# Optimization experiments

Hardware: AMD Instinct MI355X
Metric: run time of the kernel (lower is better)

Reference implementation:

```python
import jax, jax.numpy as jnp
import numpy as np

H = 64  # hidden size
IN = 1  # input size


def setup_inputs() -> dict:
    key = jax.random.key(0)
    ks = jax.random.split(key, 8)
    B, T = 4096, 512
    s_ih = 1.0 / np.sqrt(H)
    return {
        "x": jax.random.normal(ks[0], (B, T, IN), dtype=jnp.float32),
        # PyTorch LSTM params, gate order (i, f, g, o)
        "W_ih": jax.random.uniform(ks[1], (4 * H, IN), jnp.float32, -s_ih, s_ih),
        "W_hh": jax.random.uniform(ks[2], (4 * H, H), jnp.float32, -s_ih, s_ih),
        "b_ih": jax.random.uniform(ks[3], (4 * H,), jnp.float32, -s_ih, s_ih),
        "b_hh": jax.random.uniform(ks[4], (4 * H,), jnp.float32, -s_ih, s_ih),
        "W_fc": jax.random.uniform(ks[5], (1, H), jnp.float32, -s_ih, s_ih),
        "b_fc": jax.random.uniform(ks[6], (1,), jnp.float32, -s_ih, s_ih),
    }


def reference(x, W_ih, W_hh, b_ih, b_hh, W_fc, b_fc):
    B = x.shape[0]
    b = b_ih + b_hh  # fused bias, [4H]

    def step(carry, xt):
        h, c = carry  # [B,H], [B,H]
        gates = xt @ W_ih.T + h @ W_hh.T + b  # [B,4H]
        i, f, g, o = jnp.split(gates, 4, axis=-1)
        i = jax.nn.sigmoid(i)
        f = jax.nn.sigmoid(f)
        g = jnp.tanh(g)
        o = jax.nn.sigmoid(o)
        c = f * c + i * g
        h = o * jnp.tanh(c)
        return (h, c), None

    h0 = jnp.zeros((B, H), dtype=x.dtype)
    c0 = jnp.zeros((B, H), dtype=x.dtype)
    xs = jnp.swapaxes(x, 0, 1)  # [T,B,IN]
    (h_last, _), _ = jax.lax.scan(step, (h0, c0), xs)
    # fc applied to out[:, -1, :] == h_last
    return h_last @ W_fc.T + b_fc  # [B,1]
```

## Files before the change

### kernel.cpp

```cpp
#include <hip/hip_runtime.h>

#define T_STEPS 512
#define BT 16
#define XSTRIDE 524
#define HS2 136

typedef __attribute__((ext_vector_type(8))) short bf16x8;
typedef __attribute__((ext_vector_type(4))) float f32x4;
typedef __attribute__((ext_vector_type(4))) unsigned u32x4;

__device__ __forceinline__ short f2bf(float f) {
    union { float f; unsigned u; } v; v.f = f;
    unsigned r = v.u + 0x7fffu + ((v.u >> 16) & 1u);
    return (short)(r >> 16);
}
__device__ __forceinline__ float bf2f(short s) {
    union { float f; unsigned u; } v;
    v.u = ((unsigned)(unsigned short)s) << 16;
    return v.f;
}
__device__ __forceinline__ float ubits(unsigned u) {
    union { unsigned u; float f; } v; v.u = u; return v.f;
}
__device__ __forceinline__ float exp2_fast(float x) {
#if __has_builtin(__builtin_amdgcn_exp2f)
    return __builtin_amdgcn_exp2f(x);
#else
    return __expf(x * 0.69314718056f);
#endif
}

#define L2E 1.44269504089f
#define C2  2.88539008178f

__global__ __launch_bounds__(256, 1) void lstm_persist(
    const float* __restrict__ x,
    const float* __restrict__ W_ih,
    const float* __restrict__ W_hh,
    const float* __restrict__ b_ih,
    const float* __restrict__ b_hh,
    const float* __restrict__ W_fc,
    const float* __restrict__ b_fc,
    float* __restrict__ out)
{
    __shared__ __align__(16) float x_lds[BT * XSTRIDE];
    __shared__ __align__(16) short hbuf[2][BT][HS2];

    const int tid  = threadIdx.x;
    const int wave = tid >> 6;
    const int lane = tid & 63;
    const int l15  = lane & 15;
    const int quad = lane >> 4;
    const int b0   = blockIdx.x * BT;

    {
        const float* xg = x + (size_t)b0 * T_STEPS;
        #pragma unroll
        for (int i = 0; i < 8; ++i) {
            int f4 = tid + i * 256;
            int b  = f4 >> 7;
            int t4 = f4 & 127;
            float4 v = reinterpret_cast<const float4*>(xg + (size_t)b * T_STEPS)[t4];
            reinterpret_cast<float4*>(&x_lds[b * XSTRIDE + t4 * 4])[0] = v;
        }
    }
    {
        short* p = &hbuf[0][0][0];
        for (int i = tid; i < BT * HS2; i += 256) p[i] = 0;
        if (tid < BT) x_lds[tid * XSTRIDE + 512] = 0.f;
        if (tid >= 256 - 3 * BT && tid < 256) {
            int b = (tid - (256 - 3 * BT)) / 3, j = (tid - (256 - 3 * BT)) % 3;
            x_lds[b * XSTRIDE + 513 + j] = 0.f;
        }
    }

    const float scg[4] = { -L2E, -L2E, -C2, -L2E };
    bf16x8 Wv[4][4];
    f32x4 bias4[4], wih4[4];
    #pragma unroll
    for (int g = 0; g < 4; ++g) {
        int na = g * 64 + wave * 16 + l15;
        #pragma unroll
        for (int j = 0; j < 4; ++j) {
            int m = (wave + j) & 3;
            const float* wr = W_hh + na * 64 + m * 16 + quad * 4;
            bf16x8 a;
            #pragma unroll
            for (int jj = 0; jj < 4; ++jj) {
                short h16 = f2bf(wr[jj] * scg[g]);
                a[jj]     = h16;
                a[jj + 4] = h16;
            }
            Wv[g][j] = a;
        }
        #pragma unroll
        for (int r = 0; r < 4; ++r) {
            int n = g * 64 + wave * 16 + quad * 4 + r;
            bias4[g][r] = scg[g] * (b_ih[n] + b_hh[n]);
            wih4[g][r]  = scg[g] * W_ih[n];
        }
    }

    f32x4 ct4 = {0.f, 0.f, 0.f, 0.f};
    const int hoff = l15 * HS2 + quad * 8;
    const int off1 = hoff + 32 * ((wave + 1) & 3);
    const int off2 = hoff + 32 * ((wave + 2) & 3);
    const int off3 = hoff + 32 * ((wave + 3) & 3);
    const int w32  = l15 * (HS2 / 2) + (wave * 4 + quad) * 4;
    const f32x4* xrow4 = reinterpret_cast<const f32x4*>(&x_lds[l15 * XSTRIDE]);

    const f32x4 vone  = {1.f, 1.f, 1.f, 1.f};
    const f32x4 vnC2  = {-C2, -C2, -C2, -C2};
    const f32x4 vC2   = {C2, C2, C2, C2};
    const f32x4 v40   = {40.f, 40.f, 40.f, 40.f};

    u32x4 hw = {0u, 0u, 0u, 0u};

    __syncthreads();

    f32x4 xq = xrow4[0];
    f32x4 iv[4];
    {
        f32x4 xv4 = {xq[0], xq[0], xq[0], xq[0]};
        #pragma unroll
        for (int g = 0; g < 4; ++g)
            iv[g] = __builtin_elementwise_fma(wih4[g], xv4, bias4[g]);
    }

    for (int tg = 0; tg < T_STEPS / 4; ++tg) {
        f32x4 xqn = xrow4[tg + 1];
        #pragma unroll
        for (int u = 0; u < 4; ++u) {
            const int rb = u & 1, wb = rb ^ 1;
            const short* hb = &hbuf[rb][0][0];

            bf16x8 b1 = *reinterpret_cast<const bf16x8*>(hb + off1);
            bf16x8 b2 = *reinterpret_cast<const bf16x8*>(hb + off2);
            bf16x8 b3 = *reinterpret_cast<const bf16x8*>(hb + off3);
            bf16x8 bself;
            __builtin_memcpy(&bself, &hw, 16);

            f32x4 acc[4];
            #pragma unroll
            for (int g = 0; g < 4; ++g)
                acc[g] = __builtin_amdgcn_mfma_f32_16x16x32_bf16(Wv[g][0], bself, iv[g], 0, 0, 0);
            #pragma unroll
            for (int g = 0; g < 4; ++g)
                acc[g] = __builtin_amdgcn_mfma_f32_16x16x32_bf16(Wv[g][1], b1, acc[g], 0, 0, 0);
            #pragma unroll
            for (int g = 0; g < 4; ++g)
                acc[g] = __builtin_amdgcn_mfma_f32_16x16x32_bf16(Wv[g][2], b2, acc[g], 0, 0, 0);
            #pragma unroll
            for (int g = 0; g < 4; ++g)
                acc[g] = __builtin_amdgcn_mfma_f32_16x16x32_bf16(Wv[g][3], b3, acc[g], 0, 0, 0);

            {
                float xn = (u < 3) ? xq[u + 1] : xqn[0];
                f32x4 xn4 = {xn, xn, xn, xn};
                #pragma unroll
                for (int g = 0; g < 4; ++g)
                    iv[g] = __builtin_elementwise_fma(wih4[g], xn4, bias4[g]);
            }

            f32x4 ei, ef, eg, eo;
            #pragma unroll
            for (int r = 0; r < 4; ++r) {
                ei[r] = exp2_fast(acc[0][r]);
                ef[r] = exp2_fast(acc[1][r]);
                eg[r] = exp2_fast(acc[2][r]);
                eo[r] = exp2_fast(acc[3][r]);
            }
            f32x4 Ai = vone + ei, Af = vone + ef, Ag = vone + eg, Ao = vone + eo;
            f32x4 P   = Ai * Ag;
            f32x4 PAF = P * Af;
            f32x4 rP;
            #pragma unroll
            for (int r = 0; r < 4; ++r) rP[r] = __builtin_amdgcn_rcpf(PAF[r]);
            f32x4 tg4 = __builtin_elementwise_fma(vnC2, eg, vC2);
            f32x4 num = __builtin_elementwise_fma(ct4, P, tg4 * Af);
            f32x4 cn  = num * rP;
            ct4 = cn;
            f32x4 mm = __builtin_elementwise_min(-cn, v40);
            f32x4 ec;
            #pragma unroll
            for (int r = 0; r < 4; ++r) ec[r] = exp2_fast(mm[r]);
            f32x4 tc  = vone - ec;
            f32x4 den = Ao * (vone + ec);
            f32x4 rden;
            #pragma unroll
            for (int r = 0; r < 4; ++r) rden[r] = __builtin_amdgcn_rcpf(den[r]);
            f32x4 hv = tc * rden;

            unsigned hi01, hi23, lo01, lo23;
            asm("v_cvt_pk_bf16_f32 %0, %1, %2" : "=v"(hi01) : "v"(hv[0]), "v"(hv[1]));
            asm("v_cvt_pk_bf16_f32 %0, %1, %2" : "=v"(hi23) : "v"(hv[2]), "v"(hv[3]));
            f32x4 hif = { ubits(hi01 << 16), ubits(hi01 & 0xffff0000u),
                          ubits(hi23 << 16), ubits(hi23 & 0xffff0000u) };
            f32x4 l4 = hv - hif;
            asm("v_cvt_pk_bf16_f32 %0, %1, %2" : "=v"(lo01) : "v"(l4[0]), "v"(l4[1]));
            asm("v_cvt_pk_bf16_f32 %0, %1, %2" : "=v"(lo23) : "v"(l4[2]), "v"(l4[3]));
            hw = (u32x4){ hi01, hi23, lo01, lo23 };
            *reinterpret_cast<u32x4*>(reinterpret_cast<unsigned*>(&hbuf[wb][0][0]) + w32) = hw;

            __syncthreads();
        }
        xq = xqn;
    }

    if (tid < 16) {
        int b = tid;
        float s = b_fc[0];
        #pragma unroll 4
        for (int k = 0; k < 64; ++k) {
            int blk = k >> 2, j = k & 3;
            float hv = bf2f(hbuf[0][b][blk * 8 + j]) + bf2f(hbuf[0][b][blk * 8 + 4 + j]);
            s += hv * W_fc[k];
        }
        out[b0 + b] = s;
    }
}

extern "C" void kernel_launch(void* const* d_in, const int* in_sizes, int n_in,
                              void* d_out, int out_size, void* d_ws, size_t ws_size,
                              hipStream_t stream) {
    const float* x    = (const float*)d_in[0];
    const float* W_ih = (const float*)d_in[1];
    const float* W_hh = (const float*)d_in[2];
    const float* b_ih = (const float*)d_in[3];
    const float* b_hh = (const float*)d_in[4];
    const float* W_fc = (const float*)d_in[5];
    const float* b_fc = (const float*)d_in[6];
    float* out = (float*)d_out;
    const int B = in_sizes[0] / T_STEPS;
    lstm_persist<<<dim3(B / BT), dim3(256), 0, stream>>>(
        x, W_ih, W_hh, b_ih, b_hh, W_fc, b_fc, out);
}
```

Before: 313.1 us.

## Switch recurrent matmul from split-bf16 hi/lo to single fp16 MFMA

Replaces the bf16 hi+lo split representation of h (which needed K=128 across 4 MFMA chains per gate) with a single fp16 copy of h, halving the MFMA count per step to two per gate. It also simplifies h packing and the LDS layout, and drops the register-held self block. The trade is lower precision for h and W in fp16 compared with the hi/lo bf16 pair, which could affect accuracy over 512 steps.

```diff
diff --git a/kernel.cpp b/kernel.cpp
--- a/kernel.cpp
+++ b/kernel.cpp
@@ -3,22 +3,12 @@
 #define T_STEPS 512
 #define BT 16
 #define XSTRIDE 524
-#define HS2 136
-
-typedef __attribute__((ext_vector_type(8))) short bf16x8;
+#define HSTRIDE 72
+
+typedef __attribute__((ext_vector_type(8))) _Float16 f16x8;
+typedef __attribute__((ext_vector_type(4))) _Float16 f16x4;
 typedef __attribute__((ext_vector_type(4))) float f32x4;
-typedef __attribute__((ext_vector_type(4))) unsigned u32x4;
-
-__device__ __forceinline__ short f2bf(float f) {
-    union { float f; unsigned u; } v; v.f = f;
-    unsigned r = v.u + 0x7fffu + ((v.u >> 16) & 1u);
-    return (short)(r >> 16);
-}
-__device__ __forceinline__ float bf2f(short s) {
-    union { float f; unsigned u; } v;
-    v.u = ((unsigned)(unsigned short)s) << 16;
-    return v.f;
-}
+
 __device__ __forceinline__ float ubits(unsigned u) {
     union { unsigned u; float f; } v; v.u = u; return v.f;
 }
@@ -44,7 +34,7 @@
     float* __restrict__ out)
 {
     __shared__ __align__(16) float x_lds[BT * XSTRIDE];
-    __shared__ __align__(16) short hbuf[2][BT][HS2];
+    __shared__ __align__(16) _Float16 hbuf[2][BT][HSTRIDE];
 
     const int tid  = threadIdx.x;
     const int wave = tid >> 6;
@@ -65,33 +55,29 @@
         }
     }
     {
-        short* p = &hbuf[0][0][0];
-        for (int i = tid; i < BT * HS2; i += 256) p[i] = 0;
-        if (tid < BT) x_lds[tid * XSTRIDE + 512] = 0.f;
-        if (tid >= 256 - 3 * BT && tid < 256) {
-            int b = (tid - (256 - 3 * BT)) / 3, j = (tid - (256 - 3 * BT)) % 3;
-            x_lds[b * XSTRIDE + 513 + j] = 0.f;
+        _Float16* p = &hbuf[0][0][0];
+        for (int i = tid; i < BT * HSTRIDE; i += 256) p[i] = (_Float16)0.f;
+        if (tid < BT) {
+            x_lds[tid * XSTRIDE + 512] = 0.f;
+            x_lds[tid * XSTRIDE + 513] = 0.f;
+            x_lds[tid * XSTRIDE + 514] = 0.f;
+            x_lds[tid * XSTRIDE + 515] = 0.f;
         }
     }
 
     const float scg[4] = { -L2E, -L2E, -C2, -L2E };
-    bf16x8 Wv[4][4];
+    f16x8 Wf[4][2];
     f32x4 bias4[4], wih4[4];
     #pragma unroll
     for (int g = 0; g < 4; ++g) {
         int na = g * 64 + wave * 16 + l15;
         #pragma unroll
-        for (int j = 0; j < 4; ++j) {
-            int m = (wave + j) & 3;
-            const float* wr = W_hh + na * 64 + m * 16 + quad * 4;
-            bf16x8 a;
-            #pragma unroll
-            for (int jj = 0; jj < 4; ++jj) {
-                short h16 = f2bf(wr[jj] * scg[g]);
-                a[jj]     = h16;
-                a[jj + 4] = h16;
-            }
-            Wv[g][j] = a;
+        for (int m = 0; m < 2; ++m) {
+            const float* wr = W_hh + na * 64 + m * 32 + quad * 8;
+            f16x8 a;
+            #pragma unroll
+            for (int j = 0; j < 8; ++j) a[j] = (_Float16)(wr[j] * scg[g]);
+            Wf[g][m] = a;
         }
         #pragma unroll
         for (int r = 0; r < 4; ++r) {
@@ -102,11 +88,8 @@
     }
 
     f32x4 ct4 = {0.f, 0.f, 0.f, 0.f};
-    const int hoff = l15 * HS2 + quad * 8;
-    const int off1 = hoff + 32 * ((wave + 1) & 3);
-    const int off2 = hoff + 32 * ((wave + 2) & 3);
-    const int off3 = hoff + 32 * ((wave + 3) & 3);
-    const int w32  = l15 * (HS2 / 2) + (wave * 4 + quad) * 4;
+    const int hoff = l15 * HSTRIDE + quad * 8;
+    const int wofs = l15 * HSTRIDE + wave * 16 + quad * 4;
     const f32x4* xrow4 = reinterpret_cast<const f32x4*>(&x_lds[l15 * XSTRIDE]);
 
     const f32x4 vone  = {1.f, 1.f, 1.f, 1.f};
@@ -114,8 +97,6 @@
     const f32x4 vC2   = {C2, C2, C2, C2};
     const f32x4 v40   = {40.f, 40.f, 40.f, 40.f};
 
-    u32x4 hw = {0u, 0u, 0u, 0u};
-
     __syncthreads();
 
     f32x4 xq = xrow4[0];
@@ -132,27 +113,18 @@
         #pragma unroll
         for (int u = 0; u < 4; ++u) {
             const int rb = u & 1, wb = rb ^ 1;
-            const short* hb = &hbuf[rb][0][0];
-
-            bf16x8 b1 = *reinterpret_cast<const bf16x8*>(hb + off1);
-            bf16x8 b2 = *reinterpret_cast<const bf16x8*>(hb + off2);
-            bf16x8 b3 = *reinterpret_cast<const bf16x8*>(hb + off3);
-            bf16x8 bself;
-            __builtin_memcpy(&bself, &hw, 16);
+            const _Float16* hb = &hbuf[rb][0][0];
+
+            f16x8 bm0 = *reinterpret_cast<const f16x8*>(hb + hoff);
+            f16x8 bm1 = *reinterpret_cast<const f16x8*>(hb + hoff + 32);
 
             f32x4 acc[4];
             #pragma unroll
             for (int g = 0; g < 4; ++g)
-                acc[g] = __builtin_amdgcn_mfma_f32_16x16x32_bf16(Wv[g][0], bself, iv[g], 0, 0, 0);
+                acc[g] = __builtin_amdgcn_mfma_f32_16x16x32_f16(Wf[g][0], bm0, iv[g], 0, 0, 0);
             #pragma unroll
             for (int g = 0; g < 4; ++g)
-                acc[g] = __builtin_amdgcn_mfma_f32_16x16x32_bf16(Wv[g][1], b1, acc[g], 0, 0, 0);
-            #pragma unroll
-            for (int g = 0; g < 4; ++g)
-                acc[g] = __builtin_amdgcn_mfma_f32_16x16x32_bf16(Wv[g][2], b2, acc[g], 0, 0, 0);
-            #pragma unroll
-            for (int g = 0; g < 4; ++g)
-                acc[g] = __builtin_amdgcn_mfma_f32_16x16x32_bf16(Wv[g][3], b3, acc[g], 0, 0, 0);
+                acc[g] = __builtin_amdgcn_mfma_f32_16x16x32_f16(Wf[g][1], bm1, acc[g], 0, 0, 0);
 
             {
                 float xn = (u < 3) ? xq[u + 1] : xqn[0];
@@ -191,16 +163,9 @@
             for (int r = 0; r < 4; ++r) rden[r] = __builtin_amdgcn_rcpf(den[r]);
             f32x4 hv = tc * rden;
 
-            unsigned hi01, hi23, lo01, lo23;
-            asm("v_cvt_pk_bf16_f32 %0, %1, %2" : "=v"(hi01) : "v"(hv[0]), "v"(hv[1]));
-            asm("v_cvt_pk_bf16_f32 %0, %1, %2" : "=v"(hi23) : "v"(hv[2]), "v"(hv[3]));
-            f32x4 hif = { ubits(hi01 << 16), ubits(hi01 & 0xffff0000u),
-                          ubits(hi23 << 16), ubits(hi23 & 0xffff0000u) };
-            f32x4 l4 = hv - hif;
-            asm("v_cvt_pk_bf16_f32 %0, %1, %2" : "=v"(lo01) : "v"(l4[0]), "v"(l4[1]));
-            asm("v_cvt_pk_bf16_f32 %0, %1, %2" : "=v"(lo23) : "v"(l4[2]), "v"(l4[3]));
-            hw = (u32x4){ hi01, hi23, lo01, lo23 };
-            *reinterpret_cast<u32x4*>(reinterpret_cast<unsigned*>(&hbuf[wb][0][0]) + w32) = hw;
+            f16x4 h16 = { (_Float16)hv[0], (_Float16)hv[1],
+                          (_Float16)hv[2], (_Float16)hv[3] };
+            *reinterpret_cast<f16x4*>(&hbuf[wb][0][0] + wofs) = h16;
 
             __syncthreads();
         }
@@ -212,9 +177,7 @@
         float s = b_fc[0];
         #pragma unroll 4
         for (int k = 0; k < 64; ++k) {
-            int blk = k >> 2, j = k & 3;
-            float hv = bf2f(hbuf[0][b][blk * 8 + j]) + bf2f(hbuf[0][b][blk * 8 + 4 + j]);
-            s += hv * W_fc[k];
+            s += (float)hbuf[0][b][k] * W_fc[k];
         }
         out[b0 + b] = s;
     }
```

Result: faster. 268.2 us (-14.3%).
